# Performance work log

Hardware: AMD Instinct MI355X
Metric: run time of the kernel (lower is better)

The kernel has to match this reference:

```python
import jax, jax.numpy as jnp
import numpy as np
import math


def get_slopes(n_heads: int) -> jnp.ndarray:
    """ALiBi head-specific slopes, matching the torch reference."""
    n = 2 ** int(math.floor(math.log2(n_heads)))
    m0 = 2.0 ** (-8.0 / n)
    m = m0 ** jnp.arange(1, n + 1, dtype=jnp.float32)
    if n < n_heads:
        mh0 = 2.0 ** (-4.0 / n)
        mh = mh0 ** jnp.arange(1, 1 + 2 * (n_heads - n), 2, dtype=jnp.float32)
        m = jnp.concatenate([m, mh])
    return m.reshape(1, -1, 1, 1)  # [1, h, 1, 1]


def setup_inputs() -> dict:
    key = jax.random.key(0)
    kq, kk, kv, kb = jax.random.split(key, 4)
    b, h, s_q, s_kv, d = 2, 16, 2048, 2048, 128
    return {
        "query": jax.random.normal(kq, (b, h, s_q, d), dtype=jnp.float32),
        "key": jax.random.normal(kk, (b, h, s_kv, d), dtype=jnp.float32),
        "value": jax.random.normal(kv, (b, h, s_kv, d), dtype=jnp.float32),
        "bias": jax.random.normal(kb, (1, 1, s_q, s_kv), dtype=jnp.float32),
        "is_causal": 1,
        "is_infer": 0,
        "is_alibi": 1,
    }


def reference(query, key, value, bias, is_causal, is_infer, is_alibi):
    _, h, s_q, d = query.shape
    s_kv = key.shape[2]
    attn_scale = 1.0 / math.sqrt(d)

    # S = Q K^T * scale, in fp32 (matches S.to(torch.float32))
    S = jnp.einsum("bhqd,bhkd->bhqk", query, key).astype(jnp.float32) * attn_scale

    if bias is not None:
        S = S + bias

    if is_alibi:
        # relative position (k - q) scaled by per-head slope
        rel = jnp.arange(s_kv, dtype=jnp.float32) - jnp.arange(s_q, dtype=jnp.float32)[:, None]
        S = S + rel * get_slopes(h)

    if is_causal:
        causal_mask = jnp.triu(jnp.ones((s_q, s_kv), dtype=bool), k=1)
        S = jnp.where(causal_mask, -jnp.inf, S)

    Stats = None
    if not is_infer:
        row_max = jnp.max(S, axis=-1, keepdims=True)
        row_sum = jnp.sum(jnp.exp(S - row_max), axis=-1, keepdims=True)
        Stats = row_max + jnp.log(row_sum)  # logsumexp, [b,h,s_q,1]

    P = jax.nn.softmax(S, axis=-1).astype(value.dtype)
    O = jnp.einsum("bhqk,bhkd->bhqd", P, value)
    return (O, Stats)
```

## Files before the change

### kernel.cpp

```cpp
#include <hip/hip_runtime.h>
#include <hip/hip_bf16.h>
#include <math.h>

typedef __bf16 bf16;
typedef __attribute__((ext_vector_type(8))) __bf16 bf16x8;
typedef __attribute__((ext_vector_type(4))) __bf16 bf16x4;
typedef __attribute__((ext_vector_type(4))) float f32x4;

constexpr int NB = 2, NH = 16, SQ = 2048, SKV = 2048, DH = 128;
constexpr int QB = 128, KVB = 64;
constexpr float SM_SCALE = 0.08838834764831845f;
constexpr float LOG2E = 1.4426950408889634f;
constexpr float DEFER_THR = 7.0f;

#define GLD_LDS(g, l) __builtin_amdgcn_global_load_lds( \
    (const __attribute__((address_space(1))) void*)(g), \
    (__attribute__((address_space(3))) void*)(l), 16, 0, 0)

__global__ __launch_bounds__(256)
void cvt_k_kernel(const float* __restrict__ src, bf16* __restrict__ dst) {
    const size_t i = ((size_t)blockIdx.x * 256 + threadIdx.x) * 8;
    float4 a = *(const float4*)(src + i);
    float4 b = *(const float4*)(src + i + 4);
    bf16x8 f;
    f[0]=(bf16)a.x; f[1]=(bf16)a.y; f[2]=(bf16)a.z; f[3]=(bf16)a.w;
    f[4]=(bf16)b.x; f[5]=(bf16)b.y; f[6]=(bf16)b.z; f[7]=(bf16)b.w;
    *(bf16x8*)(dst + i) = f;
}

__global__ __launch_bounds__(256)
void tr_v_kernel(const float* __restrict__ src, bf16* __restrict__ dst) {
    __shared__ float Tl[64][65];
    const int bh  = blockIdx.y;
    const int kv0 = (int)(blockIdx.x >> 1) * 64;
    const int d0  = (int)(blockIdx.x & 1) * 64;
    const int t   = threadIdx.x;
    const float* sp = src + (size_t)bh * SQ * DH;
#pragma unroll
    for (int i = 0; i < 4; ++i) {
        const int row = i * 16 + (t >> 4);
        const int c4  = (t & 15) * 4;
        *(float4*)&Tl[row][c4] = *(const float4*)(sp + (size_t)(kv0 + row) * DH + d0 + c4);
    }
    __syncthreads();
    bf16* dp = dst + (size_t)bh * DH * SKV;
#pragma unroll
    for (int i = 0; i < 4; ++i) {
        const int d  = i * 16 + (t >> 4);
        const int k4 = (t & 15) * 4;
        bf16x4 o;
        o[0]=(bf16)Tl[k4+0][d]; o[1]=(bf16)Tl[k4+1][d];
        o[2]=(bf16)Tl[k4+2][d]; o[3]=(bf16)Tl[k4+3][d];
        *(bf16x4*)(dp + (size_t)(d0 + d) * SKV + kv0 + k4) = o;
    }
}

__global__ __launch_bounds__(512, 4)
void attn_fwd_kernel(const float* __restrict__ Qg, const bf16* __restrict__ Kb,
                     const bf16* __restrict__ Vb, const float* __restrict__ Bg,
                     float* __restrict__ Og, float* __restrict__ Sg)
{
    __shared__ __attribute__((aligned(16))) bf16 Kl[2][KVB * DH];
    __shared__ __attribute__((aligned(16))) bf16 Vt[2][DH * KVB];

    const int tid = threadIdx.x;
    const int w   = tid >> 6;
    const int ln  = tid & 63;
    const int l4  = ln >> 4;
    const int lm  = ln & 15;

    const int bh = blockIdx.x;
    const int h  = bh & (NH - 1);
    const int qt = (blockIdx.y < 8) ? (int)blockIdx.y : 23 - (int)blockIdx.y;
    const int q0 = qt * QB;
    const int qw = q0 + w * 16;
    const int qr = qw + lm;

    const float slope = exp2f(-0.5f * (float)(h + 1));
    const bf16* kbase = Kb + (size_t)bh * SKV * DH;
    const bf16* vbase = Vb + (size_t)bh * DH * SKV;
    const float* bprow = Bg + (size_t)qr * SKV + 8 * l4;

    int ksrc[2], vsrc[2];
#pragma unroll
    for (int i = 0; i < 2; ++i) {
        const int seg = w * 2 + i;
        const int rl  = seg * 4 + (ln >> 4);
        const int sig = ((rl >> 5) & 1) * 32 + ((rl >> 2) & 3) * 8 + ((rl >> 4) & 1) * 4 + (rl & 3);
        ksrc[i] = sig * DH + (((ln & 15) ^ (rl & 7)) << 3);
        const int d = seg * 8 + (ln >> 3);
        vsrc[i] = d * SKV + (((ln & 7) ^ (d & 7)) << 3);
    }

    auto stage = [&](int kv0n, int buf) {
#pragma unroll
        for (int i = 0; i < 2; ++i)
            GLD_LDS(kbase + (size_t)kv0n * DH + ksrc[i], &Kl[buf][(w * 2 + i) * 4 * DH]);
#pragma unroll
        for (int i = 0; i < 2; ++i)
            GLD_LDS(vbase + (size_t)kv0n + vsrc[i], &Vt[buf][(w * 2 + i) * 8 * KVB]);
    };

    bf16x8 qf[4];
    {
        const float* qrow = Qg + (size_t)bh * SQ * DH + (size_t)qr * DH;
#pragma unroll
        for (int c = 0; c < 4; ++c) {
            const float* qp = qrow + c * 32 + l4 * 8;
            float4 a = *(const float4*)qp;
            float4 b = *(const float4*)(qp + 4);
            bf16x8 f;
            f[0]=(bf16)(a.x*SM_SCALE); f[1]=(bf16)(a.y*SM_SCALE);
            f[2]=(bf16)(a.z*SM_SCALE); f[3]=(bf16)(a.w*SM_SCALE);
            f[4]=(bf16)(b.x*SM_SCALE); f[5]=(bf16)(b.y*SM_SCALE);
            f[6]=(bf16)(b.z*SM_SCALE); f[7]=(bf16)(b.w*SM_SCALE);
            qf[c] = f;
        }
    }

    bf16x8 ones;
#pragma unroll
    for (int i = 0; i < 8; ++i) ones[i] = (bf16)1.0f;

    f32x4 acc[8];
#pragma unroll
    for (int dt = 0; dt < 8; ++dt) acc[dt] = (f32x4){0.f, 0.f, 0.f, 0.f};
    f32x4 accl = (f32x4){0.f, 0.f, 0.f, 0.f};
    float mrow = -INFINITY;

    const int ntile = (q0 + QB) / KVB;

    stage(0, 0);
    f32x4 bvf[2][2];
#pragma unroll
    for (int a2 = 0; a2 < 2; ++a2)
#pragma unroll
        for (int b2 = 0; b2 < 2; ++b2)
            bvf[a2][b2] = *(const f32x4*)(bprow + a2 * 32 + b2 * 4);
    __syncthreads();
    int cur = 0;

    for (int t = 0; t < ntile; ++t) {
        const int kv0 = t * KVB;
        if (t + 1 < ntile) stage(kv0 + KVB, cur ^ 1);

        f32x4 s[4];
#pragma unroll
        for (int m = 0; m < 4; ++m) s[m] = (f32x4){0.f, 0.f, 0.f, 0.f};
        __builtin_amdgcn_s_setprio(1);
#pragma unroll
        for (int c = 0; c < 4; ++c) {
#pragma unroll
            for (int m = 0; m < 4; ++m) {
                bf16x8 kb = *(const bf16x8*)&Kl[cur][(m * 16 + lm) * DH +
                                ((((c << 2) + l4) ^ (lm & 7)) << 3)];
                s[m] = __builtin_amdgcn_mfma_f32_16x16x32_bf16(kb, qf[c], s[m], 0, 0, 0);
            }
        }
        __builtin_amdgcn_s_setprio(0);

        const int dqi = qr - kv0 - 8 * l4;
        const float base = slope * (float)(-dqi);
        float p[4][4];
        const bool needMask = (kv0 + KVB - 1 > qw);
        if (needMask) {
#pragma unroll
            for (int m = 0; m < 4; ++m) {
                const int a2 = m >> 1, b2 = m & 1;
#pragma unroll
                for (int r = 0; r < 4; ++r) {
                    const int koff = a2 * 32 + b2 * 4 + r;
                    float x = s[m][r] + bvf[a2][b2][r] + fmaf(slope, (float)koff, base);
                    p[m][r] = (koff > dqi) ? -INFINITY : x;
                }
            }
        } else {
#pragma unroll
            for (int m = 0; m < 4; ++m) {
                const int a2 = m >> 1, b2 = m & 1;
#pragma unroll
                for (int r = 0; r < 4; ++r) {
                    const int koff = a2 * 32 + b2 * 4 + r;
                    p[m][r] = s[m][r] + bvf[a2][b2][r] + fmaf(slope, (float)koff, base);
                }
            }
        }

        float mxm[4];
#pragma unroll
        for (int m = 0; m < 4; ++m)
            mxm[m] = fmaxf(fmaxf(p[m][0], p[m][1]), fmaxf(p[m][2], p[m][3]));
        float mx = fmaxf(fmaxf(mxm[0], mxm[1]), fmaxf(mxm[2], mxm[3]));
        mx = fmaxf(mx, __shfl_xor(mx, 16));
        mx = fmaxf(mx, __shfl_xor(mx, 32));

        if (__any(mx > mrow + DEFER_THR)) {
            const float mn = fmaxf(mrow, mx);
            const float al = exp2f((mrow - mn) * LOG2E);
            mrow = mn;
#pragma unroll
            for (int dt = 0; dt < 8; ++dt) {
                f32x4 a = acc[dt];
                a[0] *= al; a[1] *= al; a[2] *= al; a[3] *= al;
                acc[dt] = a;
            }
            accl[0] *= al; accl[1] *= al; accl[2] *= al; accl[3] *= al;
        }

#pragma unroll
        for (int m = 0; m < 4; ++m)
#pragma unroll
            for (int r = 0; r < 4; ++r)
                p[m][r] = exp2f((p[m][r] - mrow) * LOG2E);

        if (t + 1 < ntile) {
#pragma unroll
            for (int a2 = 0; a2 < 2; ++a2)
#pragma unroll
                for (int b2 = 0; b2 < 2; ++b2)
                    bvf[a2][b2] = *(const f32x4*)(bprow + (kv0 + KVB) + a2 * 32 + b2 * 4);
        }

        __builtin_amdgcn_s_setprio(1);
#pragma unroll
        for (int c = 0; c < 2; ++c) {
            bf16x8 pb;
            pb[0]=(bf16)p[2*c][0];   pb[1]=(bf16)p[2*c][1];
            pb[2]=(bf16)p[2*c][2];   pb[3]=(bf16)p[2*c][3];
            pb[4]=(bf16)p[2*c+1][0]; pb[5]=(bf16)p[2*c+1][1];
            pb[6]=(bf16)p[2*c+1][2]; pb[7]=(bf16)p[2*c+1][3];
            accl = __builtin_amdgcn_mfma_f32_16x16x32_bf16(ones, pb, accl, 0, 0, 0);
#pragma unroll
            for (int dt = 0; dt < 8; ++dt) {
                bf16x8 vb = *(const bf16x8*)&Vt[cur][(dt * 16 + lm) * KVB +
                                ((((c << 2) + l4) ^ (lm & 7)) << 3)];
                acc[dt] = __builtin_amdgcn_mfma_f32_16x16x32_bf16(vb, pb, acc[dt], 0, 0, 0);
            }
        }
        __builtin_amdgcn_s_setprio(0);

        __syncthreads();
        cur ^= 1;
    }

    {
        const float inv = 1.0f / accl[0];
        float* orow = Og + (size_t)bh * SQ * DH + (size_t)qr * DH;
#pragma unroll
        for (int dt = 0; dt < 8; ++dt) {
            f32x4 o = acc[dt];
            o[0] *= inv; o[1] *= inv; o[2] *= inv; o[3] *= inv;
            *(f32x4*)(orow + dt * 16 + l4 * 4) = o;
        }
    }
    if (l4 == 0)
        Sg[(size_t)bh * SQ + qr] = mrow + logf(accl[0]);
}

extern "C" void kernel_launch(void* const* d_in, const int* in_sizes, int n_in,
                              void* d_out, int out_size, void* d_ws, size_t ws_size,
                              hipStream_t stream) {
    const float* Q = (const float*)d_in[0];
    const float* K = (const float*)d_in[1];
    const float* V = (const float*)d_in[2];
    const float* B = (const float*)d_in[3];
    float* O     = (float*)d_out;
    float* Stats = O + (size_t)NB * NH * SQ * DH;

    const size_t nkv = (size_t)NB * NH * SKV * DH;
    bf16* Kb = (bf16*)d_ws;
    bf16* Vt = Kb + nkv;

    cvt_k_kernel<<<(int)(nkv / (256 * 8)), 256, 0, stream>>>(K, Kb);
    tr_v_kernel<<<dim3(64, NB * NH), 256, 0, stream>>>(V, Vt);

    dim3 grid(NB * NH, SQ / QB);
    attn_fwd_kernel<<<grid, 512, 0, stream>>>(Q, Kb, Vt, B, O, Stats);
}
```

Measured before the change: 109.6 us.

## Switch attention kernel to 32x32x16 MFMA with 4 waves of 32 query rows

Restructures the attention kernel to use 32x32x16 bf16 MFMA tiles, with 256-thread blocks where each wave owns 32 query rows instead of 16. The row-sum denominator is now accumulated with VALU adds instead of an MFMA against a ones vector. P is packed with cvt_pk_bf16 and permlane32_swap to form the B operand. The LDS swizzle for K and V is reworked, and fully masked KV tiles are skipped per wave. This aims to cut MFMA instruction count, LDS reads per FLOP and wasted causal work. In exchange it halves the waves per block and raises register pressure.

```diff
diff --git a/kernel.cpp b/kernel.cpp
--- a/kernel.cpp
+++ b/kernel.cpp
@@ -6,6 +6,8 @@
 typedef __attribute__((ext_vector_type(8))) __bf16 bf16x8;
 typedef __attribute__((ext_vector_type(4))) __bf16 bf16x4;
 typedef __attribute__((ext_vector_type(4))) float f32x4;
+typedef __attribute__((ext_vector_type(16))) float f32x16;
+typedef __attribute__((ext_vector_type(4))) unsigned int u32x4;
 
 constexpr int NB = 2, NH = 16, SQ = 2048, SKV = 2048, DH = 128;
 constexpr int QB = 128, KVB = 64;
@@ -16,6 +18,15 @@
 #define GLD_LDS(g, l) __builtin_amdgcn_global_load_lds( \
     (const __attribute__((address_space(1))) void*)(g), \
     (__attribute__((address_space(3))) void*)(l), 16, 0, 0)
+
+__device__ __forceinline__ unsigned cvt_pk_bf16(float lo, float hi) {
+    unsigned r;
+    asm("v_cvt_pk_bf16_f32 %0, %1, %2" : "=v"(r) : "v"(lo), "v"(hi));
+    return r;
+}
+__device__ __forceinline__ void permswap(unsigned &a, unsigned &b) {
+    asm("v_permlane32_swap_b32 %0, %1" : "+v"(a), "+v"(b));
+}
 
 __global__ __launch_bounds__(256)
 void cvt_k_kernel(const float* __restrict__ src, bf16* __restrict__ dst) {
@@ -55,58 +66,58 @@
     }
 }
 
-__global__ __launch_bounds__(512, 4)
+__global__ __launch_bounds__(256, 2)
 void attn_fwd_kernel(const float* __restrict__ Qg, const bf16* __restrict__ Kb,
                      const bf16* __restrict__ Vb, const float* __restrict__ Bg,
                      float* __restrict__ Og, float* __restrict__ Sg)
 {
     __shared__ __attribute__((aligned(16))) bf16 Kl[2][KVB * DH];
-    __shared__ __attribute__((aligned(16))) bf16 Vt[2][DH * KVB];
+    __shared__ __attribute__((aligned(16))) bf16 Vl[2][KVB * DH];
 
     const int tid = threadIdx.x;
     const int w   = tid >> 6;
     const int ln  = tid & 63;
-    const int l4  = ln >> 4;
-    const int lm  = ln & 15;
+    const int q5  = ln & 31;
+    const int hi  = ln >> 5;
+    const int l15 = ln & 15;
 
     const int bh = blockIdx.x;
     const int h  = bh & (NH - 1);
     const int qt = (blockIdx.y < 8) ? (int)blockIdx.y : 23 - (int)blockIdx.y;
     const int q0 = qt * QB;
-    const int qw = q0 + w * 16;
-    const int qr = qw + lm;
+    const int qw = q0 + w * 32;
+    const int qr = qw + q5;
 
     const float slope = exp2f(-0.5f * (float)(h + 1));
     const bf16* kbase = Kb + (size_t)bh * SKV * DH;
     const bf16* vbase = Vb + (size_t)bh * DH * SKV;
-    const float* bprow = Bg + (size_t)qr * SKV + 8 * l4;
-
-    int ksrc[2], vsrc[2];
-#pragma unroll
-    for (int i = 0; i < 2; ++i) {
-        const int seg = w * 2 + i;
-        const int rl  = seg * 4 + (ln >> 4);
-        const int sig = ((rl >> 5) & 1) * 32 + ((rl >> 2) & 3) * 8 + ((rl >> 4) & 1) * 4 + (rl & 3);
-        ksrc[i] = sig * DH + (((ln & 15) ^ (rl & 7)) << 3);
-        const int d = seg * 8 + (ln >> 3);
-        vsrc[i] = d * SKV + (((ln & 7) ^ (d & 7)) << 3);
+    const float* bprow = Bg + (size_t)qr * SKV + 4 * hi;
+
+    int ksrc[4], vsrc[4];
+#pragma unroll
+    for (int i = 0; i < 4; ++i) {
+        const int seg = w * 4 + i;
+        const int r   = seg * 4 + (ln >> 4);
+        const int sl  = l15 ^ (r & 15);
+        ksrc[i] = r * DH + (sl << 3);
+        vsrc[i] = (2 * r + (sl >> 3)) * SKV + ((sl & 7) << 3);
     }
 
     auto stage = [&](int kv0n, int buf) {
 #pragma unroll
-        for (int i = 0; i < 2; ++i)
-            GLD_LDS(kbase + (size_t)kv0n * DH + ksrc[i], &Kl[buf][(w * 2 + i) * 4 * DH]);
-#pragma unroll
-        for (int i = 0; i < 2; ++i)
-            GLD_LDS(vbase + (size_t)kv0n + vsrc[i], &Vt[buf][(w * 2 + i) * 8 * KVB]);
+        for (int i = 0; i < 4; ++i)
+            GLD_LDS(kbase + (size_t)kv0n * DH + ksrc[i], &Kl[buf][(w * 4 + i) * 512]);
+#pragma unroll
+        for (int i = 0; i < 4; ++i)
+            GLD_LDS(vbase + (size_t)kv0n + vsrc[i], &Vl[buf][(w * 4 + i) * 512]);
     };
 
-    bf16x8 qf[4];
+    bf16x8 qf[8];
     {
         const float* qrow = Qg + (size_t)bh * SQ * DH + (size_t)qr * DH;
 #pragma unroll
-        for (int c = 0; c < 4; ++c) {
-            const float* qp = qrow + c * 32 + l4 * 8;
+        for (int s = 0; s < 8; ++s) {
+            const float* qp = qrow + s * 16 + hi * 8;
             float4 a = *(const float4*)qp;
             float4 b = *(const float4*)(qp + 4);
             bf16x8 f;
@@ -114,29 +125,27 @@
             f[2]=(bf16)(a.z*SM_SCALE); f[3]=(bf16)(a.w*SM_SCALE);
             f[4]=(bf16)(b.x*SM_SCALE); f[5]=(bf16)(b.y*SM_SCALE);
             f[6]=(bf16)(b.z*SM_SCALE); f[7]=(bf16)(b.w*SM_SCALE);
-            qf[c] = f;
+            qf[s] = f;
         }
     }
 
-    bf16x8 ones;
-#pragma unroll
-    for (int i = 0; i < 8; ++i) ones[i] = (bf16)1.0f;
-
-    f32x4 acc[8];
-#pragma unroll
-    for (int dt = 0; dt < 8; ++dt) acc[dt] = (f32x4){0.f, 0.f, 0.f, 0.f};
-    f32x4 accl = (f32x4){0.f, 0.f, 0.f, 0.f};
+    f32x16 acc[4];
+#pragma unroll
+    for (int dt = 0; dt < 4; ++dt)
+#pragma unroll
+        for (int e = 0; e < 16; ++e) acc[dt][e] = 0.f;
+    float denom = 0.f;
     float mrow = -INFINITY;
 
     const int ntile = (q0 + QB) / KVB;
 
     stage(0, 0);
-    f32x4 bvf[2][2];
-#pragma unroll
-    for (int a2 = 0; a2 < 2; ++a2)
-#pragma unroll
-        for (int b2 = 0; b2 < 2; ++b2)
-            bvf[a2][b2] = *(const f32x4*)(bprow + a2 * 32 + b2 * 4);
+    f32x4 bvf[2][4];
+#pragma unroll
+    for (int T = 0; T < 2; ++T)
+#pragma unroll
+        for (int u = 0; u < 4; ++u)
+            bvf[T][u] = *(const f32x4*)(bprow + T * 32 + u * 8);
     __syncthreads();
     int cur = 0;
 
@@ -144,117 +153,133 @@
         const int kv0 = t * KVB;
         if (t + 1 < ntile) stage(kv0 + KVB, cur ^ 1);
 
-        f32x4 s[4];
-#pragma unroll
-        for (int m = 0; m < 4; ++m) s[m] = (f32x4){0.f, 0.f, 0.f, 0.f};
-        __builtin_amdgcn_s_setprio(1);
-#pragma unroll
-        for (int c = 0; c < 4; ++c) {
-#pragma unroll
-            for (int m = 0; m < 4; ++m) {
-                bf16x8 kb = *(const bf16x8*)&Kl[cur][(m * 16 + lm) * DH +
-                                ((((c << 2) + l4) ^ (lm & 7)) << 3)];
-                s[m] = __builtin_amdgcn_mfma_f32_16x16x32_bf16(kb, qf[c], s[m], 0, 0, 0);
-            }
+        const bool liveTile = (kv0 <= qw + 31);
+        float p[2][16];
+        if (liveTile) {
+            f32x16 s0, s1;
+#pragma unroll
+            for (int e = 0; e < 16; ++e) { s0[e] = 0.f; s1[e] = 0.f; }
+            __builtin_amdgcn_s_setprio(1);
+#pragma unroll
+            for (int s = 0; s < 8; ++s) {
+                const int sl = (((2 * s + hi) ^ l15) << 3);
+                bf16x8 k0 = *(const bf16x8*)&Kl[cur][q5 * DH + sl];
+                bf16x8 k1 = *(const bf16x8*)&Kl[cur][(32 + q5) * DH + sl];
+                s0 = __builtin_amdgcn_mfma_f32_32x32x16_bf16(k0, qf[s], s0, 0, 0, 0);
+                s1 = __builtin_amdgcn_mfma_f32_32x32x16_bf16(k1, qf[s], s1, 0, 0, 0);
+            }
+            __builtin_amdgcn_s_setprio(0);
+
+            const int dq2 = qr - kv0 - 4 * hi;
+            const float base2 = slope * (float)(-dq2);
+            const bool needMask = (kv0 + KVB - 1 > qw);
+            if (needMask) {
+#pragma unroll
+                for (int r = 0; r < 16; ++r) {
+                    const int u = r >> 2, v = r & 3;
+                    const int k0c = 8 * u + v;
+                    const int k1c = 32 + 8 * u + v;
+                    float x0 = s0[r] + bvf[0][u][v] + fmaf(slope, (float)k0c, base2);
+                    float x1 = s1[r] + bvf[1][u][v] + fmaf(slope, (float)k1c, base2);
+                    p[0][r] = (k0c > dq2) ? -INFINITY : x0;
+                    p[1][r] = (k1c > dq2) ? -INFINITY : x1;
+                }
+            } else {
+#pragma unroll
+                for (int r = 0; r < 16; ++r) {
+                    const int u = r >> 2, v = r & 3;
+                    p[0][r] = s0[r] + bvf[0][u][v] + fmaf(slope, (float)(8*u+v), base2);
+                    p[1][r] = s1[r] + bvf[1][u][v] + fmaf(slope, (float)(32+8*u+v), base2);
+                }
+            }
+
+            float mt[8];
+#pragma unroll
+            for (int r = 0; r < 8; ++r)
+                mt[r] = fmaxf(fmaxf(p[0][r], p[0][r + 8]), fmaxf(p[1][r], p[1][r + 8]));
+            float mx = fmaxf(fmaxf(fmaxf(mt[0], mt[1]), fmaxf(mt[2], mt[3])),
+                             fmaxf(fmaxf(mt[4], mt[5]), fmaxf(mt[6], mt[7])));
+            mx = fmaxf(mx, __shfl_xor(mx, 32));
+
+            if (__any(mx > mrow + DEFER_THR)) {
+                const float mn = fmaxf(mrow, mx);
+                const float al = exp2f((mrow - mn) * LOG2E);
+                mrow = mn;
+#pragma unroll
+                for (int dt = 0; dt < 4; ++dt)
+#pragma unroll
+                    for (int e = 0; e < 16; ++e) acc[dt][e] *= al;
+                denom *= al;
+            }
+
+#pragma unroll
+            for (int T = 0; T < 2; ++T)
+#pragma unroll
+                for (int r = 0; r < 16; ++r)
+                    p[T][r] = exp2f((p[T][r] - mrow) * LOG2E);
+
+            float st[8];
+#pragma unroll
+            for (int r = 0; r < 8; ++r)
+                st[r] = (p[0][r] + p[0][r + 8]) + (p[1][r] + p[1][r + 8]);
+            denom += ((st[0] + st[1]) + (st[2] + st[3])) +
+                     ((st[4] + st[5]) + (st[6] + st[7]));
         }
-        __builtin_amdgcn_s_setprio(0);
-
-        const int dqi = qr - kv0 - 8 * l4;
-        const float base = slope * (float)(-dqi);
-        float p[4][4];
-        const bool needMask = (kv0 + KVB - 1 > qw);
-        if (needMask) {
-#pragma unroll
-            for (int m = 0; m < 4; ++m) {
-                const int a2 = m >> 1, b2 = m & 1;
-#pragma unroll
-                for (int r = 0; r < 4; ++r) {
-                    const int koff = a2 * 32 + b2 * 4 + r;
-                    float x = s[m][r] + bvf[a2][b2][r] + fmaf(slope, (float)koff, base);
-                    p[m][r] = (koff > dqi) ? -INFINITY : x;
+
+        if (t + 1 < ntile) {
+#pragma unroll
+            for (int T = 0; T < 2; ++T)
+#pragma unroll
+                for (int u = 0; u < 4; ++u)
+                    bvf[T][u] = *(const f32x4*)(bprow + (kv0 + KVB) + T * 32 + u * 8);
+        }
+
+        if (liveTile) {
+            __builtin_amdgcn_s_setprio(1);
+#pragma unroll
+            for (int s2 = 0; s2 < 4; ++s2) {
+                const int T  = s2 >> 1;
+                const int r0 = (s2 & 1) * 8;
+                unsigned x1 = cvt_pk_bf16(p[T][r0 + 0], p[T][r0 + 1]);
+                unsigned x2 = cvt_pk_bf16(p[T][r0 + 2], p[T][r0 + 3]);
+                unsigned y1 = cvt_pk_bf16(p[T][r0 + 4], p[T][r0 + 5]);
+                unsigned y2 = cvt_pk_bf16(p[T][r0 + 6], p[T][r0 + 7]);
+                permswap(x1, y1);
+                permswap(x2, y2);
+                u32x4 pw; pw[0] = x1; pw[1] = x2; pw[2] = y1; pw[3] = y2;
+                const bf16x8 pb = __builtin_bit_cast(bf16x8, pw);
+                const int vsl = (((((q5 & 1) << 3) | (2 * s2 + hi)) ^ (q5 >> 1)) << 3);
+#pragma unroll
+                for (int dt = 0; dt < 4; ++dt) {
+                    bf16x8 vb = *(const bf16x8*)&Vl[cur][(dt * 16 + (q5 >> 1)) * DH + vsl];
+                    acc[dt] = __builtin_amdgcn_mfma_f32_32x32x16_bf16(vb, pb, acc[dt], 0, 0, 0);
                 }
             }
-        } else {
-#pragma unroll
-            for (int m = 0; m < 4; ++m) {
-                const int a2 = m >> 1, b2 = m & 1;
-#pragma unroll
-                for (int r = 0; r < 4; ++r) {
-                    const int koff = a2 * 32 + b2 * 4 + r;
-                    p[m][r] = s[m][r] + bvf[a2][b2][r] + fmaf(slope, (float)koff, base);
-                }
-            }
+            __builtin_amdgcn_s_setprio(0);
         }
-
-        float mxm[4];
-#pragma unroll
-        for (int m = 0; m < 4; ++m)
-            mxm[m] = fmaxf(fmaxf(p[m][0], p[m][1]), fmaxf(p[m][2], p[m][3]));
-        float mx = fmaxf(fmaxf(mxm[0], mxm[1]), fmaxf(mxm[2], mxm[3]));
-        mx = fmaxf(mx, __shfl_xor(mx, 16));
-        mx = fmaxf(mx, __shfl_xor(mx, 32));
-
-        if (__any(mx > mrow + DEFER_THR)) {
-            const float mn = fmaxf(mrow, mx);
-            const float al = exp2f((mrow - mn) * LOG2E);
-            mrow = mn;
-#pragma unroll
-            for (int dt = 0; dt < 8; ++dt) {
-                f32x4 a = acc[dt];
-                a[0] *= al; a[1] *= al; a[2] *= al; a[3] *= al;
-                acc[dt] = a;
-            }
-            accl[0] *= al; accl[1] *= al; accl[2] *= al; accl[3] *= al;
-        }
-
-#pragma unroll
-        for (int m = 0; m < 4; ++m)
-#pragma unroll
-            for (int r = 0; r < 4; ++r)
-                p[m][r] = exp2f((p[m][r] - mrow) * LOG2E);
-
-        if (t + 1 < ntile) {
-#pragma unroll
-            for (int a2 = 0; a2 < 2; ++a2)
-#pragma unroll
-                for (int b2 = 0; b2 < 2; ++b2)
-                    bvf[a2][b2] = *(const f32x4*)(bprow + (kv0 + KVB) + a2 * 32 + b2 * 4);
-        }
-
-        __builtin_amdgcn_s_setprio(1);
-#pragma unroll
-        for (int c = 0; c < 2; ++c) {
-            bf16x8 pb;
-            pb[0]=(bf16)p[2*c][0];   pb[1]=(bf16)p[2*c][1];
-            pb[2]=(bf16)p[2*c][2];   pb[3]=(bf16)p[2*c][3];
-            pb[4]=(bf16)p[2*c+1][0]; pb[5]=(bf16)p[2*c+1][1];
-            pb[6]=(bf16)p[2*c+1][2]; pb[7]=(bf16)p[2*c+1][3];
-            accl = __builtin_amdgcn_mfma_f32_16x16x32_bf16(ones, pb, accl, 0, 0, 0);
-#pragma unroll
-            for (int dt = 0; dt < 8; ++dt) {
-                bf16x8 vb = *(const bf16x8*)&Vt[cur][(dt * 16 + lm) * KVB +
-                                ((((c << 2) + l4) ^ (lm & 7)) << 3)];
-                acc[dt] = __builtin_amdgcn_mfma_f32_16x16x32_bf16(vb, pb, acc[dt], 0, 0, 0);
-            }
-        }
-        __builtin_amdgcn_s_setprio(0);
 
         __syncthreads();
         cur ^= 1;
     }
 
     {
-        const float inv = 1.0f / accl[0];
+        const float dtot = denom + __shfl_xor(denom, 32);
+        const float inv = 1.0f / dtot;
         float* orow = Og + (size_t)bh * SQ * DH + (size_t)qr * DH;
 #pragma unroll
-        for (int dt = 0; dt < 8; ++dt) {
-            f32x4 o = acc[dt];
-            o[0] *= inv; o[1] *= inv; o[2] *= inv; o[3] *= inv;
-            *(f32x4*)(orow + dt * 16 + l4 * 4) = o;
-        }
-    }
-    if (l4 == 0)
-        Sg[(size_t)bh * SQ + qr] = mrow + logf(accl[0]);
+        for (int dt = 0; dt < 4; ++dt)
+#pragma unroll
+            for (int u = 0; u < 4; ++u) {
+                f32x4 o;
+                o[0] = acc[dt][4 * u + 0] * inv;
+                o[1] = acc[dt][4 * u + 1] * inv;
+                o[2] = acc[dt][4 * u + 2] * inv;
+                o[3] = acc[dt][4 * u + 3] * inv;
+                *(f32x4*)(orow + dt * 32 + u * 8 + hi * 4) = o;
+            }
+        if (hi == 0)
+            Sg[(size_t)bh * SQ + qr] = mrow + logf(dtot);
+    }
 }
 
 extern "C" void kernel_launch(void* const* d_in, const int* in_sizes, int n_in,
@@ -275,5 +300,5 @@
     tr_v_kernel<<<dim3(64, NB * NH), 256, 0, stream>>>(V, Vt);
 
     dim3 grid(NB * NH, SQ / QB);
-    attn_fwd_kernel<<<grid, 512, 0, stream>>>(Q, Kb, Vt, B, O, Stats);
-}
+    attn_fwd_kernel<<<grid, 256, 0, stream>>>(Q, Kb, Vt, B, O, Stats);
+}
```

Measured after the change: 121.1 us. 1.1x slower.
